# Performance work log

Measured on AMD Instinct MI355X. Metric: run time of the kernel, lower is better.

## Reference

```python
import jax, jax.numpy as jnp
import numpy as np

B, S, D, H = 2, 2048, 1024, 16
HD = D // H  # head dim = 64


def setup_inputs() -> dict:
    key = jax.random.key(0)
    ks = jax.random.split(key, 11)
    s = 0.02
    return {
        "query": jax.random.normal(ks[0], (B, S, D), jnp.float32),
        "key": jax.random.normal(ks[1], (B, S, D), jnp.float32),
        "value": jax.random.normal(ks[2], (B, S, D), jnp.float32),
        "Wq": jax.random.normal(ks[3], (D, D), jnp.float32) * s,
        "bq": jnp.zeros((D,), jnp.float32),
        "Wk": jax.random.normal(ks[4], (D, D), jnp.float32) * s,
        "bk": jnp.zeros((D,), jnp.float32),
        "Wv": jax.random.normal(ks[5], (D, D), jnp.float32) * s,
        "bv": jnp.zeros((D,), jnp.float32),
        "Wo": jax.random.normal(ks[6], (D, D), jnp.float32) * s,
        "bo": jnp.zeros((D,), jnp.float32),
    }


def reference(query, key, value, Wq, bq, Wk, bk, Wv, bv, Wo, bo):
    # Linear projections (torch Linear: x @ W^T + b; here W stored as [in, out])
    q = query @ Wq + bq  # [B,S,D]
    k = key @ Wk + bk
    v = value @ Wv + bv
    # split heads -> [B,H,S,HD]
    q = q.reshape(B, S, H, HD).transpose(0, 2, 1, 3)
    k = k.reshape(B, S, H, HD).transpose(0, 2, 1, 3)
    v = v.reshape(B, S, H, HD).transpose(0, 2, 1, 3)
    scores = jnp.einsum("bhqd,bhkd->bhqk", q, k) / jnp.sqrt(jnp.float32(HD))
    probs = jax.nn.softmax(scores, axis=-1)
    # dropout is identity at inference
    ctx = jnp.einsum("bhqk,bhkd->bhqd", probs, v)
    ctx = ctx.transpose(0, 2, 1, 3).reshape(B, S, D)
    return ctx @ Wo + bo
```

## Files before the change

kernel.cpp:

```cpp
#include <hip/hip_runtime.h>
#include <hip/hip_bf16.h>

#define BB 2
#define SS 2048
#define DD 1024
#define HH 16
#define HD 64
#define MM (BB*SS)

typedef __attribute__((ext_vector_type(8))) short bf16x8;
typedef __attribute__((ext_vector_type(4))) float f32x4;

static __device__ inline unsigned short f2bf(float x) {
    unsigned int u = __float_as_uint(x);
    unsigned int r = (u + 0x7fffu + ((u >> 16) & 1u)) >> 16;
    return (unsigned short)r;
}

static __device__ inline unsigned pack2bf(float lo, float hi) {
    union { __hip_bfloat162 h; unsigned u; } c;
    c.h = __float22bfloat162_rn(make_float2(lo, hi));
    return c.u;
}

static __device__ inline f32x4 mfma16(bf16x8 a, bf16x8 b, f32x4 c) {
    return __builtin_amdgcn_mfma_f32_16x16x32_bf16(a, b, c, 0, 0, 0);
}

static __device__ inline float fast_exp2(float x) {
    return __builtin_amdgcn_exp2f(x);
}

typedef __attribute__((address_space(3))) unsigned int lds_u32;
typedef const __attribute__((address_space(1))) unsigned int glb_u32;
static __device__ inline void async_ld16(const void* g, void* l) {
    __builtin_amdgcn_global_load_lds((glb_u32*)g, (lds_u32*)l, 16, 0, 0);
}

struct PrepArgs {
    const float* csrc[3];
    unsigned short* cdst[3];
    const float* wsrc[4];
    unsigned short* wdst[4];
};
__global__ __launch_bounds__(256) void prep_inputs(PrepArgs args) {
    const int z = blockIdx.z;
    const int t = threadIdx.x;
    if (z < 3) {
        const float* in = args.csrc[z];
        unsigned short* out = args.cdst[z];
        int chunk = (blockIdx.y * 32 + blockIdx.x) * 4096;
#pragma unroll
        for (int r = 0; r < 4; r++) {
            int i = chunk + r * 1024 + t * 4;
            float4 v = *(const float4*)(in + i);
            uint2 o;
            o.x = pack2bf(v.x, v.y);
            o.y = pack2bf(v.z, v.w);
            *(uint2*)(out + i) = o;
        }
    } else {
        __shared__ float tile[32][33];
        const float* in = args.wsrc[z - 3];
        unsigned short* out = args.wdst[z - 3];
        int c0 = blockIdx.x * 32, r0 = blockIdx.y * 32;
        int x = t & 31, y0 = t >> 5;
        for (int yy = y0; yy < 32; yy += 8)
            tile[yy][x] = in[(size_t)(r0 + yy) * DD + c0 + x];
        __syncthreads();
        for (int yy = y0; yy < 32; yy += 8)
            out[(size_t)(c0 + yy) * DD + r0 + x] = f2bf(tile[x][yy]);
    }
}

__device__ inline void cstore(float* C, size_t idx, float v) { C[idx] = v; }
__device__ inline void cstore(unsigned short* C, size_t idx, float v) { C[idx] = f2bf(v); }

template <typename OutT>
__device__ inline void gemm_bt_body(const unsigned short* __restrict__ A,
                                    const unsigned short* __restrict__ Bt,
                                    const float* __restrict__ bias,
                                    OutT* __restrict__ C,
                                    int M, int N, int K, float scale, int vt) {
    __shared__ alignas(16) unsigned short As[128 * 32];
    __shared__ alignas(16) unsigned short Bs[128 * 32];
    const int t = threadIdx.x;
    const int lane = t & 63, wave = t >> 6;
    const int quad = lane >> 4, l15 = lane & 15;
    const int wm = wave & 1, wn = wave >> 1;
    const int m0 = blockIdx.y * 128, n0 = blockIdx.x * 128;

    const unsigned short* gA = A + (size_t)(m0 + wave * 32 + (lane >> 2)) * K + (lane & 3) * 8;
    const unsigned short* gB = Bt + (size_t)(n0 + wave * 32 + (lane >> 2)) * K + (lane & 3) * 8;
    unsigned short* lA0 = &As[(wave * 32) * 32];
    unsigned short* lA1 = &As[(wave * 32 + 16) * 32];
    unsigned short* lB0 = &Bs[(wave * 32) * 32];
    unsigned short* lB1 = &Bs[(wave * 32 + 16) * 32];

    f32x4 acc[4][4];
#pragma unroll
    for (int i = 0; i < 4; i++)
#pragma unroll
        for (int j = 0; j < 4; j++) acc[i][j] = (f32x4){0.f, 0.f, 0.f, 0.f};

    for (int k0 = 0; k0 < K; k0 += 32) {
        __syncthreads();
        async_ld16(gA + k0, lA0);
        async_ld16(gA + (size_t)16 * K + k0, lA1);
        async_ld16(gB + k0, lB0);
        async_ld16(gB + (size_t)16 * K + k0, lB1);
        __syncthreads();

        bf16x8 af[4], bfr[4];
#pragma unroll
        for (int i = 0; i < 4; i++)
            af[i] = *(const bf16x8*)&As[(wm * 64 + i * 16 + l15) * 32 + quad * 8];
#pragma unroll
        for (int j = 0; j < 4; j++)
            bfr[j] = *(const bf16x8*)&Bs[(wn * 64 + j * 16 + l15) * 32 + quad * 8];
#pragma unroll
        for (int i = 0; i < 4; i++)
#pragma unroll
            for (int j = 0; j < 4; j++)
                acc[i][j] = mfma16(af[i], bfr[j], acc[i][j]);
    }

    if (vt) {
#pragma unroll
        for (int j = 0; j < 4; j++) {
            int col = n0 + wn * 64 + j * 16 + l15;
            float bv = bias[col];
#pragma unroll
            for (int i = 0; i < 4; i++) {
                int rowb = m0 + wm * 64 + i * 16 + quad * 4;
                int b = rowb >> 11, s = rowb & (SS - 1);
                uint2 w;
                w.x = pack2bf(acc[i][j][0] + bv, acc[i][j][1] + bv);
                w.y = pack2bf(acc[i][j][2] + bv, acc[i][j][3] + bv);
                *(uint2*)((unsigned short*)C + (size_t)b * DD * SS + (size_t)col * SS + s) = w;
            }
        }
    } else {
#pragma unroll
        for (int j = 0; j < 4; j++) {
            int col = n0 + wn * 64 + j * 16 + l15;
            float bv = bias[col];
#pragma unroll
            for (int i = 0; i < 4; i++) {
                int rowb = m0 + wm * 64 + i * 16 + quad * 4;
#pragma unroll
                for (int rr = 0; rr < 4; rr++) {
                    float v = (acc[i][j][rr] + bv) * scale;
                    cstore(C, (size_t)(rowb + rr) * N + col, v);
                }
            }
        }
    }
}

struct QKVArgs {
    const unsigned short* A[3];
    const unsigned short* Bt[3];
    const float* bias[3];
    unsigned short* C[3];
};

#define QSCALE 0.1803368801111204f

__global__ __launch_bounds__(256) void gemm_qkv(QKVArgs args) {
    int z = blockIdx.z;
    float scale = (z == 0) ? QSCALE : 1.0f;
    gemm_bt_body<unsigned short>(args.A[z], args.Bt[z], args.bias[z], args.C[z],
                                 MM, DD, DD, scale, z == 2);
}

__global__ __launch_bounds__(256) void gemm_out(const unsigned short* __restrict__ A,
                                                const unsigned short* __restrict__ Bt,
                                                const float* __restrict__ bias,
                                                float* __restrict__ C) {
    __shared__ alignas(16) unsigned short As[128 * 32];
    __shared__ alignas(16) unsigned short Bs[64 * 32];
    const int t = threadIdx.x;
    const int lane = t & 63, wave = t >> 6;
    const int quad = lane >> 4, l15 = lane & 15;
    const int m0 = blockIdx.y * 128, n0 = blockIdx.x * 64;
    const int K = DD, N = DD;

    const unsigned short* gA = A + (size_t)(m0 + wave * 16 + (lane >> 2)) * K + (lane & 3) * 8;
    const unsigned short* gB = Bt + (size_t)(n0 + wave * 16 + (lane >> 2)) * K + (lane & 3) * 8;
    unsigned short* lA0 = &As[(wave * 16) * 32];
    unsigned short* lA1 = &As[(wave * 16 + 64) * 32];
    unsigned short* lB0 = &Bs[(wave * 16) * 32];

    f32x4 acc[2][4];
#pragma unroll
    for (int i = 0; i < 2; i++)
#pragma unroll
        for (int j = 0; j < 4; j++) acc[i][j] = (f32x4){0.f, 0.f, 0.f, 0.f};

    for (int k0 = 0; k0 < K; k0 += 32) {
        __syncthreads();
        async_ld16(gA + k0, lA0);
        async_ld16(gA + (size_t)64 * K + k0, lA1);
        async_ld16(gB + k0, lB0);
        __syncthreads();

        bf16x8 af[2], bfr[4];
#pragma unroll
        for (int i = 0; i < 2; i++)
            af[i] = *(const bf16x8*)&As[(wave * 32 + i * 16 + l15) * 32 + quad * 8];
#pragma unroll
        for (int j = 0; j < 4; j++)
            bfr[j] = *(const bf16x8*)&Bs[(j * 16 + l15) * 32 + quad * 8];
#pragma unroll
        for (int i = 0; i < 2; i++)
#pragma unroll
            for (int j = 0; j < 4; j++)
                acc[i][j] = mfma16(af[i], bfr[j], acc[i][j]);
    }

#pragma unroll
    for (int j = 0; j < 4; j++) {
        int col = n0 + j * 16 + l15;
        float bv = bias[col];
#pragma unroll
        for (int i = 0; i < 2; i++) {
            int rowb = m0 + wave * 32 + i * 16 + quad * 4;
#pragma unroll
            for (int rr = 0; rr < 4; rr++)
                C[(size_t)(rowb + rr) * N + col] = acc[i][j][rr] + bv;
        }
    }
}

#define TK 64
#define NTILE (SS / TK)
#define LDP 72

__global__ __launch_bounds__(256, 2) void flash_attn(const unsigned short* __restrict__ Q,
                                                     const unsigned short* __restrict__ Kg,
                                                     const unsigned short* __restrict__ Vt,
                                                     unsigned short* __restrict__ ctx) {
    __shared__ alignas(16) unsigned short Ks[2][TK * LDP];
    __shared__ alignas(16) unsigned short Vs[2][TK * LDP];
    const int t = threadIdx.x;
    const int lane = t & 63, wave = t >> 6;
    const int quad = lane >> 4, l15 = lane & 15;
    const int qg = blockIdx.x & 15;
    const int bh = blockIdx.x >> 4;
    const int h = bh & 15, b = bh >> 4;
    const int q0 = (qg * 4 + wave) * 32;

    const unsigned short* Qb = Q + (size_t)b * SS * DD + h * HD;
    const unsigned short* Kb = Kg + (size_t)b * SS * DD + h * HD;
    const unsigned short* Vb = Vt + ((size_t)b * DD + h * HD) * SS;

    const int r0 = t >> 3, cs = t & 7;
    const unsigned short* gK = Kb + (size_t)r0 * DD + cs * 8;
    const unsigned short* gV = Vb + (size_t)r0 * SS + cs * 8;
    const int ldsoff0 = r0 * LDP + cs * 8;
    const int ldsoff1 = (r0 + 32) * LDP + cs * 8;

    bf16x8 qa[2][2];
#pragma unroll
    for (int qt = 0; qt < 2; qt++) {
        qa[qt][0] = *(const bf16x8*)(Qb + (size_t)(q0 + qt * 16 + l15) * DD + quad * 8);
        qa[qt][1] = *(const bf16x8*)(Qb + (size_t)(q0 + qt * 16 + l15) * DD + 32 + quad * 8);
    }

    float lrow[2] = {0.f, 0.f};
    f32x4 o[2][4];
#pragma unroll
    for (int qt = 0; qt < 2; qt++)
#pragma unroll
        for (int j = 0; j < 4; j++) o[qt][j] = (f32x4){0.f, 0.f, 0.f, 0.f};

    {
        uint4 kr0 = *(const uint4*)(gK);
        uint4 kr1 = *(const uint4*)(gK + (size_t)32 * DD);
        uint4 vr0 = *(const uint4*)(gV);
        uint4 vr1 = *(const uint4*)(gV + (size_t)32 * SS);
        *(uint4*)&Ks[0][ldsoff0] = kr0;
        *(uint4*)&Ks[0][ldsoff1] = kr1;
        *(uint4*)&Vs[0][ldsoff0] = vr0;
        *(uint4*)&Vs[0][ldsoff1] = vr1;
    }
    __syncthreads();

    for (int tile = 0; tile < NTILE; ++tile) {
        const int buf = tile & 1;
        uint4 kr0, kr1, vr0, vr1;
        if (tile + 1 < NTILE) {
            const unsigned short* gKn = gK + (size_t)(tile + 1) * TK * DD;
            const unsigned short* gVn = gV + (tile + 1) * TK;
            kr0 = *(const uint4*)(gKn);
            kr1 = *(const uint4*)(gKn + (size_t)32 * DD);
            vr0 = *(const uint4*)(gVn);
            vr1 = *(const uint4*)(gVn + (size_t)32 * SS);
        }
        const unsigned short* Ksb = Ks[buf];
        const unsigned short* Vsb = Vs[buf];
#pragma unroll
        for (int half = 0; half < 2; half++) {
            const int kb0 = half * 32;
            bf16x8 k0 = *(const bf16x8*)&Ksb[(kb0 + l15) * LDP + quad * 8];
            bf16x8 k1 = *(const bf16x8*)&Ksb[(kb0 + l15) * LDP + 32 + quad * 8];
            bf16x8 k2 = *(const bf16x8*)&Ksb[(kb0 + 16 + l15) * LDP + quad * 8];
            bf16x8 k3 = *(const bf16x8*)&Ksb[(kb0 + 16 + l15) * LDP + 32 + quad * 8];
            union { ushort4 s[2]; bf16x8 v; } af[4];
#pragma unroll
            for (int j = 0; j < 4; j++) {
                af[j].s[0] = *(const ushort4*)&Vsb[(j * 16 + l15) * LDP + kb0 + quad * 4];
                af[j].s[1] = *(const ushort4*)&Vsb[(j * 16 + l15) * LDP + kb0 + 16 + quad * 4];
            }
#pragma unroll
            for (int qt = 0; qt < 2; qt++) {
                f32x4 sc0 = (f32x4){0.f, 0.f, 0.f, 0.f};
                f32x4 sc1 = (f32x4){0.f, 0.f, 0.f, 0.f};
                sc0 = mfma16(k0, qa[qt][0], sc0);
                sc0 = mfma16(k1, qa[qt][1], sc0);
                sc1 = mfma16(k2, qa[qt][0], sc1);
                sc1 = mfma16(k3, qa[qt][1], sc1);

                float p[8];
#pragma unroll
                for (int rr = 0; rr < 4; rr++) {
                    p[rr]     = fast_exp2(sc0[rr]);
                    p[rr + 4] = fast_exp2(sc1[rr]);
                }
                lrow[qt] += (p[0] + p[1]) + (p[2] + p[3]) + (p[4] + p[5]) + (p[6] + p[7]);

                union { unsigned u[4]; bf16x8 v; } pf;
                pf.u[0] = pack2bf(p[0], p[1]);
                pf.u[1] = pack2bf(p[2], p[3]);
                pf.u[2] = pack2bf(p[4], p[5]);
                pf.u[3] = pack2bf(p[6], p[7]);

#pragma unroll
                for (int j = 0; j < 4; j++)
                    o[qt][j] = mfma16(af[j].v, pf.v, o[qt][j]);
            }
        }
        if (tile + 1 < NTILE) {
            __syncthreads();
            *(uint4*)&Ks[buf ^ 1][ldsoff0] = kr0;
            *(uint4*)&Ks[buf ^ 1][ldsoff1] = kr1;
            *(uint4*)&Vs[buf ^ 1][ldsoff0] = vr0;
            *(uint4*)&Vs[buf ^ 1][ldsoff1] = vr1;
            __syncthreads();
        }
    }

#pragma unroll
    for (int qt = 0; qt < 2; qt++) {
        float l = lrow[qt];
        l += __shfl_xor(l, 16, 64);
        l += __shfl_xor(l, 32, 64);
        float linv = 1.0f / l;
        unsigned short* crow = ctx + ((size_t)b * SS + q0 + qt * 16 + l15) * DD + h * HD;
#pragma unroll
        for (int j = 0; j < 4; j++) {
            uint2 w;
            w.x = pack2bf(o[qt][j][0] * linv, o[qt][j][1] * linv);
            w.y = pack2bf(o[qt][j][2] * linv, o[qt][j][3] * linv);
            *(uint2*)(crow + j * 16 + quad * 4) = w;
        }
    }
}

extern "C" void kernel_launch(void* const* d_in, const int* in_sizes, int n_in,
                              void* d_out, int out_size, void* d_ws, size_t ws_size,
                              hipStream_t stream) {
    const float* query = (const float*)d_in[0];
    const float* key   = (const float*)d_in[1];
    const float* value = (const float*)d_in[2];
    const float* Wq = (const float*)d_in[3];
    const float* bq = (const float*)d_in[4];
    const float* Wk = (const float*)d_in[5];
    const float* bk = (const float*)d_in[6];
    const float* Wv = (const float*)d_in[7];
    const float* bv = (const float*)d_in[8];
    const float* Wo = (const float*)d_in[9];
    const float* bo = (const float*)d_in[10];
    float* out = (float*)d_out;

    char* ws = (char*)d_ws;
    const size_t WSZ = (size_t)DD * DD * 2;
    const size_t XSZ = (size_t)MM * DD * 2;
    unsigned short* Wqt = (unsigned short*)(ws + 0 * WSZ);
    unsigned short* Wkt = (unsigned short*)(ws + 1 * WSZ);
    unsigned short* Wvt = (unsigned short*)(ws + 2 * WSZ);
    unsigned short* Wot = (unsigned short*)(ws + 3 * WSZ);
    unsigned short* Xq  = (unsigned short*)(ws + 4 * WSZ);
    unsigned short* Xk  = (unsigned short*)(ws + 4 * WSZ + 1 * XSZ);
    unsigned short* Xv  = (unsigned short*)(ws + 4 * WSZ + 2 * XSZ);
    unsigned short* Qp  = (unsigned short*)(ws + 4 * WSZ + 3 * XSZ);
    unsigned short* Kp  = (unsigned short*)(ws + 4 * WSZ + 4 * XSZ);
    unsigned short* Vtp = (unsigned short*)(ws + 4 * WSZ + 5 * XSZ);
    unsigned short* ctx = Xk;

    PrepArgs pargs;
    pargs.csrc[0] = query; pargs.csrc[1] = key; pargs.csrc[2] = value;
    pargs.cdst[0] = Xq; pargs.cdst[1] = Xk; pargs.cdst[2] = Xv;
    pargs.wsrc[0] = Wq; pargs.wsrc[1] = Wk; pargs.wsrc[2] = Wv; pargs.wsrc[3] = Wo;
    pargs.wdst[0] = Wqt; pargs.wdst[1] = Wkt; pargs.wdst[2] = Wvt; pargs.wdst[3] = Wot;
    prep_inputs<<<dim3(32, 32, 7), 256, 0, stream>>>(pargs);

    QKVArgs args;
    args.A[0] = Xq; args.A[1] = Xk; args.A[2] = Xv;
    args.Bt[0] = Wqt; args.Bt[1] = Wkt; args.Bt[2] = Wvt;
    args.bias[0] = bq; args.bias[1] = bk; args.bias[2] = bv;
    args.C[0] = Qp; args.C[1] = Kp; args.C[2] = Vtp;
    gemm_qkv<<<dim3(DD / 128, MM / 128, 3), 256, 0, stream>>>(args);

    flash_attn<<<BB * HH * 16, 256, 0, stream>>>(Qp, Kp, Vtp, ctx);

    gemm_out<<<dim3(DD / 64, MM / 128), 256, 0, stream>>>(ctx, Wot, bo, out);
}
```

Baseline: 243.4 us.

## Rewrite QKV GEMM with 256x256 tiles, 4-stage async LDS pipeline, swizzle

Replaces the single-buffered 128x128 QKV projection GEMM with a 512-thread 256x256 tile kernel. It uses a 4-deep ring of shared-memory buffers fed by async global-to-LDS loads with explicit vmcnt waits, so loads for upcoming k-steps overlap the current MFMAs. It also adds an XOR swizzle on the LDS slot to reduce bank conflicts and raises wave priority around the MFMA block. The costs are much higher LDS use (128 KB per block), more accumulator registers, and a grid of only 192 blocks, which may leave CUs underused.

```diff
diff --git a/kernel.cpp b/kernel.cpp
--- a/kernel.cpp
+++ b/kernel.cpp
@@ -73,91 +73,6 @@
     }
 }
 
-__device__ inline void cstore(float* C, size_t idx, float v) { C[idx] = v; }
-__device__ inline void cstore(unsigned short* C, size_t idx, float v) { C[idx] = f2bf(v); }
-
-template <typename OutT>
-__device__ inline void gemm_bt_body(const unsigned short* __restrict__ A,
-                                    const unsigned short* __restrict__ Bt,
-                                    const float* __restrict__ bias,
-                                    OutT* __restrict__ C,
-                                    int M, int N, int K, float scale, int vt) {
-    __shared__ alignas(16) unsigned short As[128 * 32];
-    __shared__ alignas(16) unsigned short Bs[128 * 32];
-    const int t = threadIdx.x;
-    const int lane = t & 63, wave = t >> 6;
-    const int quad = lane >> 4, l15 = lane & 15;
-    const int wm = wave & 1, wn = wave >> 1;
-    const int m0 = blockIdx.y * 128, n0 = blockIdx.x * 128;
-
-    const unsigned short* gA = A + (size_t)(m0 + wave * 32 + (lane >> 2)) * K + (lane & 3) * 8;
-    const unsigned short* gB = Bt + (size_t)(n0 + wave * 32 + (lane >> 2)) * K + (lane & 3) * 8;
-    unsigned short* lA0 = &As[(wave * 32) * 32];
-    unsigned short* lA1 = &As[(wave * 32 + 16) * 32];
-    unsigned short* lB0 = &Bs[(wave * 32) * 32];
-    unsigned short* lB1 = &Bs[(wave * 32 + 16) * 32];
-
-    f32x4 acc[4][4];
-#pragma unroll
-    for (int i = 0; i < 4; i++)
-#pragma unroll
-        for (int j = 0; j < 4; j++) acc[i][j] = (f32x4){0.f, 0.f, 0.f, 0.f};
-
-    for (int k0 = 0; k0 < K; k0 += 32) {
-        __syncthreads();
-        async_ld16(gA + k0, lA0);
-        async_ld16(gA + (size_t)16 * K + k0, lA1);
-        async_ld16(gB + k0, lB0);
-        async_ld16(gB + (size_t)16 * K + k0, lB1);
-        __syncthreads();
-
-        bf16x8 af[4], bfr[4];
-#pragma unroll
-        for (int i = 0; i < 4; i++)
-            af[i] = *(const bf16x8*)&As[(wm * 64 + i * 16 + l15) * 32 + quad * 8];
-#pragma unroll
-        for (int j = 0; j < 4; j++)
-            bfr[j] = *(const bf16x8*)&Bs[(wn * 64 + j * 16 + l15) * 32 + quad * 8];
-#pragma unroll
-        for (int i = 0; i < 4; i++)
-#pragma unroll
-            for (int j = 0; j < 4; j++)
-                acc[i][j] = mfma16(af[i], bfr[j], acc[i][j]);
-    }
-
-    if (vt) {
-#pragma unroll
-        for (int j = 0; j < 4; j++) {
-            int col = n0 + wn * 64 + j * 16 + l15;
-            float bv = bias[col];
-#pragma unroll
-            for (int i = 0; i < 4; i++) {
-                int rowb = m0 + wm * 64 + i * 16 + quad * 4;
-                int b = rowb >> 11, s = rowb & (SS - 1);
-                uint2 w;
-                w.x = pack2bf(acc[i][j][0] + bv, acc[i][j][1] + bv);
-                w.y = pack2bf(acc[i][j][2] + bv, acc[i][j][3] + bv);
-                *(uint2*)((unsigned short*)C + (size_t)b * DD * SS + (size_t)col * SS + s) = w;
-            }
-        }
-    } else {
-#pragma unroll
-        for (int j = 0; j < 4; j++) {
-            int col = n0 + wn * 64 + j * 16 + l15;
-            float bv = bias[col];
-#pragma unroll
-            for (int i = 0; i < 4; i++) {
-                int rowb = m0 + wm * 64 + i * 16 + quad * 4;
-#pragma unroll
-                for (int rr = 0; rr < 4; rr++) {
-                    float v = (acc[i][j][rr] + bv) * scale;
-                    cstore(C, (size_t)(rowb + rr) * N + col, v);
-                }
-            }
-        }
-    }
-}
-
 struct QKVArgs {
     const unsigned short* A[3];
     const unsigned short* Bt[3];
@@ -167,11 +82,111 @@
 
 #define QSCALE 0.1803368801111204f
 
-__global__ __launch_bounds__(256) void gemm_qkv(QKVArgs args) {
-    int z = blockIdx.z;
-    float scale = (z == 0) ? QSCALE : 1.0f;
-    gemm_bt_body<unsigned short>(args.A[z], args.Bt[z], args.bias[z], args.C[z],
-                                 MM, DD, DD, scale, z == 2);
+#define NBUF 4
+#define NT (DD / 32)
+
+__global__ __launch_bounds__(512, 2) void gemm_qkv(QKVArgs args) {
+    __shared__ alignas(16) unsigned short AS[NBUF][256 * 32];
+    __shared__ alignas(16) unsigned short BS[NBUF][256 * 32];
+    const int z = blockIdx.z;
+    const float scale = (z == 0) ? QSCALE : 1.0f;
+    const unsigned short* __restrict__ A = args.A[z];
+    const unsigned short* __restrict__ Bt = args.Bt[z];
+    const float* __restrict__ bias = args.bias[z];
+    unsigned short* __restrict__ C = args.C[z];
+    const int K = DD, N = DD;
+    const int t = threadIdx.x;
+    const int lane = t & 63, wave = t >> 6;
+    const int quad = lane >> 4, l15 = lane & 15;
+    const int wm = wave & 1, wn = wave >> 1;
+    const int m0 = blockIdx.y * 256, n0 = blockIdx.x * 256;
+
+    const int srow = wave * 16 + (lane >> 2);
+    const int sslot = (lane & 3) ^ ((lane >> 3) & 3);
+    const unsigned short* gA0 = A + (size_t)(m0 + srow) * K + sslot * 8;
+    const unsigned short* gA1 = gA0 + (size_t)128 * K;
+    const unsigned short* gB0 = Bt + (size_t)(n0 + srow) * K + sslot * 8;
+    const unsigned short* gB1 = gB0 + (size_t)128 * K;
+    const int rlo = wave * 512;
+    const int rhi = wave * 512 + 4096;
+
+    const int swzq = quad ^ ((l15 >> 1) & 3);
+
+    auto stage = [&](int kt) {
+        const int b = kt & (NBUF - 1);
+        const size_t ko = (size_t)kt * 32;
+        async_ld16(gA0 + ko, &AS[b][rlo]);
+        async_ld16(gA1 + ko, &AS[b][rhi]);
+        async_ld16(gB0 + ko, &BS[b][rlo]);
+        async_ld16(gB1 + ko, &BS[b][rhi]);
+    };
+
+    stage(0); stage(1); stage(2);
+
+    f32x4 acc[8][4];
+#pragma unroll
+    for (int i = 0; i < 8; i++)
+#pragma unroll
+        for (int j = 0; j < 4; j++) acc[i][j] = (f32x4){0.f, 0.f, 0.f, 0.f};
+
+#pragma unroll 4
+    for (int kt = 0; kt < NT; ++kt) {
+        if (kt < NT - 2)       asm volatile("s_waitcnt vmcnt(8)" ::: "memory");
+        else if (kt == NT - 2) asm volatile("s_waitcnt vmcnt(4)" ::: "memory");
+        else                   asm volatile("s_waitcnt vmcnt(0)" ::: "memory");
+        __builtin_amdgcn_s_barrier();
+        if (kt + 3 < NT) stage(kt + 3);
+
+        const unsigned short* Ab = AS[kt & (NBUF - 1)];
+        const unsigned short* Bb = BS[kt & (NBUF - 1)];
+        bf16x8 af[8], bfr[4];
+#pragma unroll
+        for (int i = 0; i < 8; i++)
+            af[i] = *(const bf16x8*)&Ab[(wm * 128 + i * 16 + l15) * 32 + swzq * 8];
+#pragma unroll
+        for (int j = 0; j < 4; j++)
+            bfr[j] = *(const bf16x8*)&Bb[(wn * 64 + j * 16 + l15) * 32 + swzq * 8];
+
+        __builtin_amdgcn_s_setprio(1);
+#pragma unroll
+        for (int i = 0; i < 8; i++)
+#pragma unroll
+            for (int j = 0; j < 4; j++)
+                acc[i][j] = mfma16(af[i], bfr[j], acc[i][j]);
+        __builtin_amdgcn_s_setprio(0);
+    }
+
+    if (z == 2) {
+#pragma unroll
+        for (int j = 0; j < 4; j++) {
+            int col = n0 + wn * 64 + j * 16 + l15;
+            float bv = bias[col];
+#pragma unroll
+            for (int i = 0; i < 8; i++) {
+                int rowb = m0 + wm * 128 + i * 16 + quad * 4;
+                int b = rowb >> 11, s = rowb & (SS - 1);
+                uint2 w;
+                w.x = pack2bf(acc[i][j][0] + bv, acc[i][j][1] + bv);
+                w.y = pack2bf(acc[i][j][2] + bv, acc[i][j][3] + bv);
+                *(uint2*)(C + (size_t)b * DD * SS + (size_t)col * SS + s) = w;
+            }
+        }
+    } else {
+#pragma unroll
+        for (int j = 0; j < 4; j++) {
+            int col = n0 + wn * 64 + j * 16 + l15;
+            float bv = bias[col];
+#pragma unroll
+            for (int i = 0; i < 8; i++) {
+                int rowb = m0 + wm * 128 + i * 16 + quad * 4;
+#pragma unroll
+                for (int rr = 0; rr < 4; rr++) {
+                    float v = (acc[i][j][rr] + bv) * scale;
+                    C[(size_t)(rowb + rr) * N + col] = f2bf(v);
+                }
+            }
+        }
+    }
 }
 
 __global__ __launch_bounds__(256) void gemm_out(const unsigned short* __restrict__ A,
@@ -411,7 +426,7 @@
     args.Bt[0] = Wqt; args.Bt[1] = Wkt; args.Bt[2] = Wvt;
     args.bias[0] = bq; args.bias[1] = bk; args.bias[2] = bv;
     args.C[0] = Qp; args.C[1] = Kp; args.C[2] = Vtp;
-    gemm_qkv<<<dim3(DD / 128, MM / 128, 3), 256, 0, stream>>>(args);
+    gemm_qkv<<<dim3(DD / 256, MM / 256, 3), 512, 0, stream>>>(args);
 
     flash_attn<<<BB * HH * 16, 256, 0, stream>>>(Qp, Kp, Vtp, ctx);
 
```

Measured after the change: 230.8 us. 1.05x faster.
